# Optimization experiments

Hardware: AMD Instinct MI355X
Metric: run time of the kernel (lower is better)

## Reference

```python
import jax, jax.numpy as jnp
import numpy as np

EPS = 1e-8


def quaternion_mul(q, m):
    # Hamilton product q * m over last dim of size 4 (w, x, y, z)
    w1, x1, y1, z1 = q[..., 0], q[..., 1], q[..., 2], q[..., 3]
    w2, x2, y2, z2 = m[..., 0], m[..., 1], m[..., 2], m[..., 3]
    return jnp.stack([
        w1 * w2 - x1 * x2 - y1 * y2 - z1 * z2,
        w1 * x2 + x1 * w2 + y1 * z2 - z1 * y2,
        w1 * y2 - x1 * z2 + y1 * w2 + z1 * x2,
        w1 * z2 + x1 * y2 - y1 * x2 + z1 * w2,
    ], axis=-1)


def quaternion_normalize(q):
    n = jnp.linalg.norm(q, axis=-1, keepdims=True)
    return q / (n + EPS)


def setup_inputs() -> dict:
    key = jax.random.key(0)
    k = jax.random.split(key, 5)
    B, S, D, H = 4, 2048, 1024, 1024
    scale = 0.02
    return {
        "x": jax.random.normal(k[0], (B, S, D), dtype=jnp.float32),
        "W_in": jax.random.normal(k[1], (3 * H, D), dtype=jnp.float32) * scale,
        "b_in": jax.random.normal(k[2], (3 * H,), dtype=jnp.float32) * scale,
        "W_out": jax.random.normal(k[3], (D, 4 * H), dtype=jnp.float32) * scale,
        "b_out": jax.random.normal(k[4], (D,), dtype=jnp.float32) * scale,
    }


def reference(x, W_in, b_in, W_out, b_out):
    B, S, D = x.shape
    H = W_in.shape[0] // 3
    # input projection -> rotation parameters v in R^3 per hidden channel
    v = (jnp.einsum('bsd,ed->bse', x, W_in) + b_in).reshape(B, S, H, 3)
    # SU(2) exponential map: v -> unit quaternion
    theta = jnp.linalg.norm(v, axis=-1, keepdims=True)          # (B,S,H,1)
    axis = v / (theta + EPS)
    q_inputs = jnp.concatenate([jnp.cos(theta), jnp.sin(theta) * axis], axis=-1)  # (B,S,H,4)

    # initial identity quaternion state (B,H,4)
    m0 = jnp.zeros((B, H, 4), dtype=x.dtype).at[..., 0].set(1.0)

    def step(m, q_t):
        m_new = quaternion_normalize(quaternion_mul(q_t, m))
        return m_new, m_new

    q_seq = jnp.transpose(q_inputs, (1, 0, 2, 3))               # (S,B,H,4)
    m_final, ms = jax.lax.scan(step, m0, q_seq)                 # ms: (S,B,H,4)

    states = jnp.transpose(ms, (1, 0, 2, 3)).reshape(B, S, 4 * H)
    full_output = jnp.einsum('bsf,df->bsd', states, W_out) + b_out
    return full_output, m_final
```

## Files before the change

### kernel.cpp

```cpp
#include <hip/hip_runtime.h>
#include <hip/hip_bf16.h>
#include <stdint.h>

#define EPSF 1e-8f

typedef __attribute__((ext_vector_type(8))) short short8;
typedef __attribute__((ext_vector_type(8))) _Float16 half8;
typedef __attribute__((ext_vector_type(4))) float floatx4;

__device__ __forceinline__ unsigned short f2h(float f) {
    _Float16 h = (_Float16)f;
    return __builtin_bit_cast(unsigned short, h);
}


__global__ void prep_kernel(const float* __restrict__ x, unsigned short* __restrict__ x16,
                            const float* __restrict__ wi, unsigned short* __restrict__ wi16,
                            const float* __restrict__ wo, unsigned short* __restrict__ wo16,
                            int nx, int nw, int nwo) {
    int i = blockIdx.x * blockDim.x + threadIdx.x;
    if (i < nx) {
        x16[i] = f2h(x[i]);
    } else if (i < nx + nw) {
        int j = i - nx;
        wi16[j] = f2h(wi[j]);
    } else if (i < nx + nw + nwo) {
        int j = i - nx - nw;
        wo16[j] = f2h(wo[j]);
    }
}


__device__ __forceinline__ void gld16(const unsigned short* g, unsigned short* l) {
    __builtin_amdgcn_global_load_lds(
        (const __attribute__((address_space(1))) unsigned int*)g,
        (__attribute__((address_space(3))) unsigned int*)l, 16, 0, 0);
}

template <int BM, int BN, int BK>
__global__ __launch_bounds__(256)
void gemm_bt(const unsigned short* __restrict__ Am, const unsigned short* __restrict__ Bm,
             const float* __restrict__ bias, float* __restrict__ C,
             int M, int N, int K) {
    constexpr int IF  = BM / 32;
    constexpr int JF  = BN / 32;
    constexpr int KH  = BK / 32;
    constexpr int CPR = BK / 8;
    extern __shared__ unsigned short smem[];
    unsigned short* sA = smem;
    unsigned short* sB = smem + BM * BK;

    const int tid  = threadIdx.x;
    const int lane = tid & 63;
    const int wid  = tid >> 6;
    const int wr   = wid >> 1, wc = wid & 1;
    const int m16  = lane & 15, quad = lane >> 4;

    const int rowA0 = blockIdx.y * BM;
    const int rowB0 = blockIdx.x * BN;

    floatx4 acc[IF][JF];
#pragma unroll
    for (int i = 0; i < IF; i++)
#pragma unroll
        for (int j = 0; j < JF; j++) acc[i][j] = (floatx4){0.f, 0.f, 0.f, 0.f};

    const int nk = K / BK;
    for (int kt = 0; kt < nk; ++kt) {
        const int k0 = kt * BK;
#pragma unroll
        for (int i = 0; i < BM * CPR / 256; i++) {
            int c = tid + 256 * i;
            int r = c / CPR, ccl = c % CPR;
            int ccg = ccl ^ (r & (CPR - 1));
            gld16(Am + (size_t)(rowA0 + r) * K + k0 + ccg * 8, sA + c * 8);
        }
#pragma unroll
        for (int i = 0; i < BN * CPR / 256; i++) {
            int c = tid + 256 * i;
            int r = c / CPR, ccl = c % CPR;
            int ccg = ccl ^ (r & (CPR - 1));
            gld16(Bm + (size_t)(rowB0 + r) * K + k0 + ccg * 8, sB + c * 8);
        }
        __syncthreads();

#pragma unroll
        for (int kh = 0; kh < KH; kh++) {
            short8 a[IF], b[JF];
            const int kc = kh * 4 + quad;
#pragma unroll
            for (int i = 0; i < IF; i++) {
                int ra = wr * (BM / 2) + i * 16 + m16;
                int pa = ra * CPR + (kc ^ (ra & (CPR - 1)));
                a[i] = *(const short8*)(sA + pa * 8);
            }
#pragma unroll
            for (int j = 0; j < JF; j++) {
                int rb = wc * (BN / 2) + j * 16 + m16;
                int pb = rb * CPR + (kc ^ (rb & (CPR - 1)));
                b[j] = *(const short8*)(sB + pb * 8);
            }
#pragma unroll
            for (int i = 0; i < IF; i++)
#pragma unroll
                for (int j = 0; j < JF; j++)
                    acc[i][j] = __builtin_amdgcn_mfma_f32_16x16x32_f16(
                        __builtin_bit_cast(half8, a[i]), __builtin_bit_cast(half8, b[j]),
                        acc[i][j], 0, 0, 0);
        }
        __syncthreads();
    }

#pragma unroll
    for (int i = 0; i < IF; i++) {
#pragma unroll
        for (int j = 0; j < JF; j++) {
            int col  = rowB0 + wc * (BN / 2) + j * 16 + m16;
            float bv = bias[col];
#pragma unroll
            for (int r = 0; r < 4; r++) {
                int row = rowA0 + wr * (BM / 2) + i * 16 + quad * 4 + r;
                C[(size_t)row * N + col] = acc[i][j][r] + bv;
            }
        }
    }
}


struct Q { float w, x, y, z; };

__device__ __forceinline__ Q qmul(Q a, Q b) {
    Q r;
    r.w = a.w * b.w - a.x * b.x - a.y * b.y - a.z * b.z;
    r.x = a.w * b.x + a.x * b.w + a.y * b.z - a.z * b.y;
    r.y = a.w * b.y - a.x * b.z + a.y * b.w + a.z * b.x;
    r.z = a.w * b.z + a.x * b.y - a.y * b.x + a.z * b.w;
    return r;
}
__device__ __forceinline__ Q qnorm(Q a) {
    float nn = a.w * a.w + a.x * a.x + a.y * a.y + a.z * a.z;
    float inv = __frsqrt_rn(nn);
    Q r; r.w = a.w * inv; r.x = a.x * inv; r.y = a.y * inv; r.z = a.z * inv;
    return r;
}
__device__ __forceinline__ Q vquat(float vx, float vy, float vz) {
    float th = sqrtf(vx * vx + vy * vy + vz * vz);
    float s_, c_;
    __sincosf(th, &s_, &c_);
    float k = __fdividef(s_, th + EPSF);
    Q q; q.w = c_; q.x = k * vx; q.y = k * vy; q.z = k * vz;
    return q;
}

#define SEG  64
#define NSEG 32

__global__ __launch_bounds__(256)
void seg_prod_kernel(const float* __restrict__ v, float* __restrict__ partials,
                     int S, int H) {
    const int b  = blockIdx.z;
    const int h  = blockIdx.y * 64 + (threadIdx.x & 63);
    const int sg = blockIdx.x * 4 + (threadIdx.x >> 6);
    const int s0 = sg * SEG;
    const size_t vstep = (size_t)3 * H;
    const float* vp = v + ((size_t)b * S + s0) * vstep + (size_t)h * 3;

    constexpr int CH = 8;
    float ax[CH], ay[CH], az[CH], bx[CH], by[CH], bz[CH];
#pragma unroll
    for (int i = 0; i < CH; ++i) {
        ax[i] = vp[i * vstep + 0]; ay[i] = vp[i * vstep + 1]; az[i] = vp[i * vstep + 2];
    }
    Q c = {1.f, 0.f, 0.f, 0.f};
    const int NC = SEG / CH;
    for (int cc = 0; cc < NC; cc += 2) {
        if (cc + 1 < NC) {
            const float* p = vp + (size_t)(cc + 1) * CH * vstep;
#pragma unroll
            for (int i = 0; i < CH; ++i) {
                bx[i] = p[i * vstep + 0]; by[i] = p[i * vstep + 1]; bz[i] = p[i * vstep + 2];
            }
        }
#pragma unroll
        for (int i = 0; i < CH; ++i) c = qmul(vquat(ax[i], ay[i], az[i]), c);
        if (cc + 2 < NC) {
            const float* p = vp + (size_t)(cc + 2) * CH * vstep;
#pragma unroll
            for (int i = 0; i < CH; ++i) {
                ax[i] = p[i * vstep + 0]; ay[i] = p[i * vstep + 1]; az[i] = p[i * vstep + 2];
            }
        }
#pragma unroll
        for (int i = 0; i < CH; ++i) c = qmul(vquat(bx[i], by[i], bz[i]), c);
    }
    float4* dst = (float4*)(partials + (((size_t)b * NSEG + sg) * H + h) * 4);
    *dst = make_float4(c.w, c.x, c.y, c.z);
}

__global__ __launch_bounds__(256)
void seg_scan_kernel(float* __restrict__ partials, float* __restrict__ m_final, int H) {
    const int t = blockIdx.x * blockDim.x + threadIdx.x;
    const int b = t >> 10, h = t & 1023;
    float4 sv[NSEG];
#pragma unroll
    for (int sg = 0; sg < NSEG; ++sg)
        sv[sg] = *(const float4*)(partials + (((size_t)b * NSEG + sg) * H + h) * 4);
    Q r = {1.f, 0.f, 0.f, 0.f};
#pragma unroll
    for (int sg = 0; sg < NSEG; ++sg) {
        *(float4*)(partials + (((size_t)b * NSEG + sg) * H + h) * 4) =
            make_float4(r.w, r.x, r.y, r.z);
        Q pq = {sv[sg].x, sv[sg].y, sv[sg].z, sv[sg].w};
        r = qmul(pq, r);
    }
    r = qnorm(r);
    float* mf = m_final + (size_t)t * 4;
    mf[0] = r.w; mf[1] = r.x; mf[2] = r.y; mf[3] = r.z;
}

__global__ __launch_bounds__(256)
void apply_kernel(const float* __restrict__ v, const float* __restrict__ pfx,
                  unsigned short* __restrict__ st, int S, int H) {
    const int b  = blockIdx.z;
    const int h  = blockIdx.y * 64 + (threadIdx.x & 63);
    const int sg = blockIdx.x * 4 + (threadIdx.x >> 6);
    const int s0 = sg * SEG;
    const size_t vstep = (size_t)3 * H;
    const size_t sstep = (size_t)4 * H;
    const float* vp = v + ((size_t)b * S + s0) * vstep + (size_t)h * 3;
    unsigned short* sp = st + ((size_t)b * S + s0) * sstep + (size_t)h * 4;

    float4 p = *(const float4*)(pfx + (((size_t)b * NSEG + sg) * H + h) * 4);
    Q R = {p.x, p.y, p.z, p.w};

    constexpr int CH = 8;
    float ax[CH], ay[CH], az[CH], bx[CH], by[CH], bz[CH];
#pragma unroll
    for (int i = 0; i < CH; ++i) {
        ax[i] = vp[i * vstep + 0]; ay[i] = vp[i * vstep + 1]; az[i] = vp[i * vstep + 2];
    }
    const int NC = SEG / CH;
    for (int cc = 0; cc < NC; cc += 2) {
        if (cc + 1 < NC) {
            const float* pp = vp + (size_t)(cc + 1) * CH * vstep;
#pragma unroll
            for (int i = 0; i < CH; ++i) {
                bx[i] = pp[i * vstep + 0]; by[i] = pp[i * vstep + 1]; bz[i] = pp[i * vstep + 2];
            }
        }
#pragma unroll
        for (int i = 0; i < CH; ++i) {
            R = qmul(vquat(ax[i], ay[i], az[i]), R);
            Q m = qnorm(R);
            ushort4 u; u.x = f2h(m.w); u.y = f2h(m.x); u.z = f2h(m.y); u.w = f2h(m.z);
            *(ushort4*)(sp + (size_t)(cc * CH + i) * sstep) = u;
        }
        if (cc + 2 < NC) {
            const float* pp = vp + (size_t)(cc + 2) * CH * vstep;
#pragma unroll
            for (int i = 0; i < CH; ++i) {
                ax[i] = pp[i * vstep + 0]; ay[i] = pp[i * vstep + 1]; az[i] = pp[i * vstep + 2];
            }
        }
#pragma unroll
        for (int i = 0; i < CH; ++i) {
            R = qmul(vquat(bx[i], by[i], bz[i]), R);
            Q m = qnorm(R);
            ushort4 u; u.x = f2h(m.w); u.y = f2h(m.x); u.z = f2h(m.y); u.w = f2h(m.z);
            *(ushort4*)(sp + (size_t)((cc + 1) * CH + i) * sstep) = u;
        }
    }
}


extern "C" void kernel_launch(void* const* d_in, const int* in_sizes, int n_in,
                              void* d_out, int out_size, void* d_ws, size_t ws_size,
                              hipStream_t stream) {
    const float* x     = (const float*)d_in[0];
    const float* W_in  = (const float*)d_in[1];
    const float* b_in  = (const float*)d_in[2];
    const float* W_out = (const float*)d_in[3];
    const float* b_out = (const float*)d_in[4];
    float* out = (float*)d_out;

    const int B = 4, S = 2048, D = 1024, H = 1024;
    const int M  = B * S;
    const int N1 = 3 * H;
    const int K1 = D;
    const int N2 = D;
    const int K2 = 4 * H;

    char* ws = (char*)d_ws;
    float*          v    = (float*)(ws);
    unsigned short* st   = (unsigned short*)(ws + 100663296u);
    unsigned short* x16  = (unsigned short*)(ws + 100663296u);
    unsigned short* wi16 = (unsigned short*)(ws + 100663296u + 16777216u);
    unsigned short* wo16 = (unsigned short*)(ws + 167772160u);

    float* partials = out;

    const int nx  = M * K1;
    const int nw  = N1 * K1;
    const int nwo = N2 * K2;
    const int ntot = nx + nw + nwo;

    prep_kernel<<<(ntot + 255) / 256, 256, 0, stream>>>(
        x, x16, W_in, wi16, W_out, wo16, nx, nw, nwo);

    gemm_bt<128, 128, 64><<<dim3(N1 / 128, M / 128), 256, 32768, stream>>>(
        x16, wi16, b_in, v, M, N1, K1);

    dim3 sg_grid(NSEG / 4, H / 64, B);
    seg_prod_kernel<<<sg_grid, 256, 0, stream>>>(v, partials, S, H);
    seg_scan_kernel<<<(B * H) / 256, 256, 0, stream>>>(partials, out + (size_t)M * D, H);
    apply_kernel<<<sg_grid, 256, 0, stream>>>(v, partials, st, S, H);

    gemm_bt<128, 128, 64><<<dim3(N2 / 128, M / 128), 256, 32768, stream>>>(
        st, wo16, b_out, out, M, N2, K2);
}
```

Baseline: 344.4 us.

## Vectorize conversion, fuse segment scan into apply, widen first GEMM tile

The fp32-to-fp16 prep kernel now loads float4 and stores ushort4, so each thread converts four elements. The separate segment-scan kernel is removed: each apply block stages all segment partials into shared memory and computes its own prefix product, and the last segment writes m_final. The first GEMM uses 128x256 tiles with more LDS, and A fragments are now loaded inside the MFMA loop to reduce register pressure. This saves a launch and a global round trip, but repeats the prefix product in every block and changes GEMM occupancy.

```diff
diff --git a/kernel.cpp b/kernel.cpp
--- a/kernel.cpp
+++ b/kernel.cpp
@@ -14,19 +14,26 @@
 }
 
 
-__global__ void prep_kernel(const float* __restrict__ x, unsigned short* __restrict__ x16,
-                            const float* __restrict__ wi, unsigned short* __restrict__ wi16,
-                            const float* __restrict__ wo, unsigned short* __restrict__ wo16,
-                            int nx, int nw, int nwo) {
+__global__ void prep_kernel(const float4* __restrict__ x4, ushort4* __restrict__ x16,
+                            const float4* __restrict__ wi4, ushort4* __restrict__ wi16,
+                            const float4* __restrict__ wo4, ushort4* __restrict__ wo16,
+                            int nx4, int nw4, int nwo4) {
     int i = blockIdx.x * blockDim.x + threadIdx.x;
-    if (i < nx) {
-        x16[i] = f2h(x[i]);
-    } else if (i < nx + nw) {
-        int j = i - nx;
-        wi16[j] = f2h(wi[j]);
-    } else if (i < nx + nw + nwo) {
-        int j = i - nx - nw;
-        wo16[j] = f2h(wo[j]);
+    float4 f; ushort4 u;
+    if (i < nx4) {
+        f = x4[i];
+        u.x = f2h(f.x); u.y = f2h(f.y); u.z = f2h(f.z); u.w = f2h(f.w);
+        x16[i] = u;
+    } else if (i < nx4 + nw4) {
+        int j = i - nx4;
+        f = wi4[j];
+        u.x = f2h(f.x); u.y = f2h(f.y); u.z = f2h(f.z); u.w = f2h(f.w);
+        wi16[j] = u;
+    } else if (i < nx4 + nw4 + nwo4) {
+        int j = i - nx4 - nw4;
+        f = wo4[j];
+        u.x = f2h(f.x); u.y = f2h(f.y); u.z = f2h(f.z); u.w = f2h(f.w);
+        wo16[j] = u;
     }
 }
 
@@ -86,14 +93,8 @@
 
 #pragma unroll
         for (int kh = 0; kh < KH; kh++) {
-            short8 a[IF], b[JF];
             const int kc = kh * 4 + quad;
-#pragma unroll
-            for (int i = 0; i < IF; i++) {
-                int ra = wr * (BM / 2) + i * 16 + m16;
-                int pa = ra * CPR + (kc ^ (ra & (CPR - 1)));
-                a[i] = *(const short8*)(sA + pa * 8);
-            }
+            short8 b[JF];
 #pragma unroll
             for (int j = 0; j < JF; j++) {
                 int rb = wc * (BN / 2) + j * 16 + m16;
@@ -101,12 +102,16 @@
                 b[j] = *(const short8*)(sB + pb * 8);
             }
 #pragma unroll
-            for (int i = 0; i < IF; i++)
+            for (int i = 0; i < IF; i++) {
+                int ra = wr * (BM / 2) + i * 16 + m16;
+                int pa = ra * CPR + (kc ^ (ra & (CPR - 1)));
+                short8 a = *(const short8*)(sA + pa * 8);
 #pragma unroll
                 for (int j = 0; j < JF; j++)
                     acc[i][j] = __builtin_amdgcn_mfma_f32_16x16x32_f16(
-                        __builtin_bit_cast(half8, a[i]), __builtin_bit_cast(half8, b[j]),
+                        __builtin_bit_cast(half8, a), __builtin_bit_cast(half8, b[j]),
                         acc[i][j], 0, 0, 0);
+            }
         }
         __syncthreads();
     }
@@ -198,40 +203,33 @@
 }
 
 __global__ __launch_bounds__(256)
-void seg_scan_kernel(float* __restrict__ partials, float* __restrict__ m_final, int H) {
-    const int t = blockIdx.x * blockDim.x + threadIdx.x;
-    const int b = t >> 10, h = t & 1023;
-    float4 sv[NSEG];
-#pragma unroll
-    for (int sg = 0; sg < NSEG; ++sg)
-        sv[sg] = *(const float4*)(partials + (((size_t)b * NSEG + sg) * H + h) * 4);
-    Q r = {1.f, 0.f, 0.f, 0.f};
-#pragma unroll
-    for (int sg = 0; sg < NSEG; ++sg) {
-        *(float4*)(partials + (((size_t)b * NSEG + sg) * H + h) * 4) =
-            make_float4(r.w, r.x, r.y, r.z);
-        Q pq = {sv[sg].x, sv[sg].y, sv[sg].z, sv[sg].w};
-        r = qmul(pq, r);
-    }
-    r = qnorm(r);
-    float* mf = m_final + (size_t)t * 4;
-    mf[0] = r.w; mf[1] = r.x; mf[2] = r.y; mf[3] = r.z;
-}
-
-__global__ __launch_bounds__(256)
-void apply_kernel(const float* __restrict__ v, const float* __restrict__ pfx,
-                  unsigned short* __restrict__ st, int S, int H) {
-    const int b  = blockIdx.z;
-    const int h  = blockIdx.y * 64 + (threadIdx.x & 63);
-    const int sg = blockIdx.x * 4 + (threadIdx.x >> 6);
-    const int s0 = sg * SEG;
+void apply_kernel(const float* __restrict__ v, const float* __restrict__ partials,
+                  unsigned short* __restrict__ st, float* __restrict__ m_final,
+                  int S, int H) {
+    const int b   = blockIdx.z;
+    const int hb  = blockIdx.y * 64;
+    const int hl  = threadIdx.x & 63;
+    const int h   = hb + hl;
+    const int sg  = blockIdx.x * 4 + (threadIdx.x >> 6);
+    const int s0  = sg * SEG;
     const size_t vstep = (size_t)3 * H;
     const size_t sstep = (size_t)4 * H;
     const float* vp = v + ((size_t)b * S + s0) * vstep + (size_t)h * 3;
     unsigned short* sp = st + ((size_t)b * S + s0) * sstep + (size_t)h * 4;
 
-    float4 p = *(const float4*)(pfx + (((size_t)b * NSEG + sg) * H + h) * 4);
-    Q R = {p.x, p.y, p.z, p.w};
+    __shared__ float4 lp[NSEG][64];
+    for (int i = threadIdx.x; i < NSEG * 64; i += 256) {
+        int s2 = i >> 6, hh = i & 63;
+        lp[s2][hh] = *(const float4*)(partials + (((size_t)b * NSEG + s2) * H + hb + hh) * 4);
+    }
+    __syncthreads();
+
+    Q R = {1.f, 0.f, 0.f, 0.f};
+    for (int s2 = 0; s2 < sg; ++s2) {
+        float4 pv = lp[s2][hl];
+        Q pq = {pv.x, pv.y, pv.z, pv.w};
+        R = qmul(pq, R);
+    }
 
     constexpr int CH = 8;
     float ax[CH], ay[CH], az[CH], bx[CH], by[CH], bz[CH];
@@ -269,6 +267,12 @@
             ushort4 u; u.x = f2h(m.w); u.y = f2h(m.x); u.z = f2h(m.y); u.w = f2h(m.z);
             *(ushort4*)(sp + (size_t)((cc + 1) * CH + i) * sstep) = u;
         }
+    }
+
+    if (sg == NSEG - 1) {
+        Q m = qnorm(R);
+        float* mf = m_final + ((size_t)b * H + h) * 4;
+        mf[0] = m.w; mf[1] = m.x; mf[2] = m.y; mf[3] = m.z;
     }
 }
 
@@ -302,18 +306,18 @@
     const int nx  = M * K1;
     const int nw  = N1 * K1;
     const int nwo = N2 * K2;
-    const int ntot = nx + nw + nwo;
-
-    prep_kernel<<<(ntot + 255) / 256, 256, 0, stream>>>(
-        x, x16, W_in, wi16, W_out, wo16, nx, nw, nwo);
-
-    gemm_bt<128, 128, 64><<<dim3(N1 / 128, M / 128), 256, 32768, stream>>>(
+    const int n4  = (nx + nw + nwo) / 4;
+
+    prep_kernel<<<(n4 + 255) / 256, 256, 0, stream>>>(
+        (const float4*)x, (ushort4*)x16, (const float4*)W_in, (ushort4*)wi16,
+        (const float4*)W_out, (ushort4*)wo16, nx / 4, nw / 4, nwo / 4);
+
+    gemm_bt<128, 256, 64><<<dim3(N1 / 256, M / 128), 256, 49152, stream>>>(
         x16, wi16, b_in, v, M, N1, K1);
 
     dim3 sg_grid(NSEG / 4, H / 64, B);
     seg_prod_kernel<<<sg_grid, 256, 0, stream>>>(v, partials, S, H);
-    seg_scan_kernel<<<(B * H) / 256, 256, 0, stream>>>(partials, out + (size_t)M * D, H);
-    apply_kernel<<<sg_grid, 256, 0, stream>>>(v, partials, st, S, H);
+    apply_kernel<<<sg_grid, 256, 0, stream>>>(v, partials, st, out + (size_t)M * D, S, H);
 
     gemm_bt<128, 128, 64><<<dim3(N2 / 128, M / 128), 256, 32768, stream>>>(
         st, wo16, b_out, out, M, N2, K2);
```

Result: no change. 348.6 us (+1.2%).
